# Kernel tuning notes

Measured on AMD Instinct MI355X. Metric: run time of the kernel, lower is better.

The kernel has to match this reference:

```python
import jax, jax.numpy as jnp
import numpy as np

N = 100000       # nodes
E = 1600000      # edges
NFEAT = 128
NHID = 128
NCLASS = 64
NHEAD = 4
NLAYER = 3
LRELU_ALPHA = 0.2


def setup_inputs() -> dict:
    key = jax.random.key(0)
    ks = jax.random.split(key, 7)
    x = jax.random.normal(ks[0], (N, NFEAT), jnp.float32)
    edge_index = jax.random.randint(ks[1], (2, E), 0, N, jnp.int32)
    # xavier-uniform-ish init scales (gain for relu baked into scale roughly)
    Win = jax.random.normal(ks[2], (NFEAT, NHID), jnp.float32) * (2.0 / (NFEAT + NHID)) ** 0.5
    b_in = jnp.zeros((NHID,), jnp.float32)
    # per hidden layer, per head: a split into (src, dst) halves of the (1, 2*in) vector
    a_hid = jax.random.normal(ks[3], (NLAYER - 1, NHEAD, 2, NHID), jnp.float32) * 0.1
    W_hid = jax.random.normal(ks[4], (NLAYER - 1, NHEAD, NHID, NHID // NHEAD), jnp.float32) * (2.0 / (NHID + NHID // NHEAD)) ** 0.5
    a_out = jax.random.normal(ks[5], (2, NHID), jnp.float32) * 0.1
    W_out = jax.random.normal(ks[6], (NHID, NCLASS), jnp.float32) * (2.0 / (NHID + NCLASS)) ** 0.5
    return dict(x=x, edge_index=edge_index, Win=Win, b_in=b_in,
                a_hid=a_hid, W_hid=W_hid, a_out=a_out, W_out=W_out)


def _segment_softmax(logits, seg, n):
    # numerically stable softmax over groups defined by seg (axis 0)
    m = jax.ops.segment_max(logits, seg, num_segments=n)
    e = jnp.exp(logits - m[seg])
    s = jax.ops.segment_sum(e, seg, num_segments=n)
    return e / s[seg]


def _gat_conv(h, row, col, a, W):
    # h: [N, D]; a: [H, 2, D]; W: [H, D, Dh]
    n = h.shape[0]
    H = a.shape[0]
    s_src = h @ a[:, 0, :].T  # [N, H]
    s_dst = h @ a[:, 1, :].T  # [N, H]
    logits = jax.nn.leaky_relu(s_src[row] + s_dst[col], LRELU_ALPHA)  # [E, H]
    alpha = _segment_softmax(logits, row, n)  # softmax grouped by row (edge_index[0])
    h_col = h[col]  # [E, D] gathered once, reused per head
    outs = []
    for hd in range(H):  # small fixed head loop keeps peak memory at [E, D]
        agg = jax.ops.segment_sum(alpha[:, hd, None] * h_col, row, num_segments=n)  # [N, D]
        outs.append(agg @ W[hd])  # weight applied AFTER aggregation, as in source
    return jnp.concatenate(outs, axis=1)


def reference(x, edge_index, Win, b_in, a_hid, W_hid, a_out, W_out):
    row, col = edge_index[0], edge_index[1]
    h = jax.nn.elu(x @ Win + b_in)  # in_linear + ELU (dropout is identity in eval/p=0)
    for l in range(a_hid.shape[0]):
        h = jax.nn.elu(_gat_conv(h, row, col, a_hid[l], W_hid[l]))
    # final conv: single head to nclass, no activation
    return _gat_conv(h, row, col, a_out[None], W_out[None])
```

## Files before the change

kernel.cpp:

```cpp
#include <hip/hip_runtime.h>
#include <hip/hip_bf16.h>
#include <cstdint>
#include <cstddef>

#define LRELU_ALPHA 0.2f
#define LOG2E 1.44269504088896f

typedef __attribute__((ext_vector_type(8))) short short8;
typedef __attribute__((ext_vector_type(4))) float f32x4;
typedef _Float16 h2v __attribute__((ext_vector_type(2)));

__device__ __forceinline__ unsigned short f2bf(float f) {
    unsigned int u = __float_as_uint(f);
    unsigned int r = (u + 0x7fffu + ((u >> 16) & 1u)) >> 16;
    return (unsigned short)r;
}
__device__ __forceinline__ float bf2f(unsigned int lo16) {
    return __uint_as_float(lo16 << 16);
}
__device__ __forceinline__ unsigned int pk2(float a, float b) {
    return (unsigned int)f2bf(a) | ((unsigned int)f2bf(b) << 16);
}
__device__ __forceinline__ float fexp2(float x) {
#if __has_builtin(__builtin_amdgcn_exp2f)
    return __builtin_amdgcn_exp2f(x);
#else
    return __expf(x * 0.69314718056f);
#endif
}
__device__ __forceinline__ h2v pkrtz(float a, float b) {
#if __has_builtin(__builtin_amdgcn_cvt_pkrtz)
    auto r = __builtin_amdgcn_cvt_pkrtz(a, b);
    union { decltype(r) i; h2v o; } u;
    u.i = r;
    return u.o;
#else
    h2v r; r.x = (_Float16)a; r.y = (_Float16)b; return r;
#endif
}
__device__ __forceinline__ unsigned int pack_lo(unsigned int a, unsigned int b) {
#if __has_builtin(__builtin_amdgcn_perm)
    return __builtin_amdgcn_perm(a, b, 0x01000504u);
#else
    return (a & 0xffffu) | (b << 16);
#endif
}
__device__ __forceinline__ unsigned int pack_hi(unsigned int a, unsigned int b) {
#if __has_builtin(__builtin_amdgcn_perm)
    return __builtin_amdgcn_perm(a, b, 0x03020706u);
#else
    return (a >> 16) | (b & 0xffff0000u);
#endif
}
union U32H2 { unsigned int u; h2v h; };
__device__ __forceinline__ float dot2f(unsigned int a, h2v w, float acc) {
    U32H2 c; c.u = a;
#if __has_builtin(__builtin_amdgcn_fdot2)
    return __builtin_amdgcn_fdot2(c.h, w, acc, false);
#else
    return acc + (float)c.h.x * (float)w.x + (float)c.h.y * (float)w.y;
#endif
}


__global__ void fill_hist_k(const int* __restrict__ ei, int* __restrict__ counts,
                            int* __restrict__ rank, int* __restrict__ scol,
                            float* __restrict__ sdA, float* __restrict__ sdB,
                            float* __restrict__ sdC, unsigned int* __restrict__ hW,
                            int N_, int E_, int total) {
    int i = blockIdx.x * 256 + threadIdx.x;
    if (i < total) scol[i] = N_;
    if (i < E_) {
        int r = ei[i];
        rank[i] = atomicAdd(&counts[r], 1);
    }
    if (blockIdx.x == 0) {
        int t = threadIdx.x;
        if (t < 4) { sdA[N_ * 4 + t] = -1e30f; sdB[N_ * 4 + t] = -1e30f; }
        if (t == 4) sdC[N_] = -1e30f;
        if (t >= 32 && t < 64)  hW[(size_t)N_ * 32 + (t - 32)] = 0u;
        if (t >= 64 && t < 128) hW[(size_t)N_ * 64 + (t - 64)] = 0u;
    }
}

__global__ void scan_block_k(const int* __restrict__ counts, int* __restrict__ tmp,
                             int* __restrict__ bsum, int n) {
    __shared__ int s[256];
    int i = blockIdx.x * 256 + threadIdx.x;
    int v = (i < n) ? ((counts[i] + 7) & ~7) : 0;
    s[threadIdx.x] = v;
    __syncthreads();
    for (int d = 1; d < 256; d <<= 1) {
        int t_ = (threadIdx.x >= d) ? s[threadIdx.x - d] : 0;
        __syncthreads();
        s[threadIdx.x] += t_;
        __syncthreads();
    }
    if (i < n) tmp[i] = s[threadIdx.x];
    if (threadIdx.x == 255) bsum[blockIdx.x] = s[255];
}

__global__ void scan_sums_k(int* bsum, int nb) {
    __shared__ int s[512];
    int v = ((int)threadIdx.x < nb) ? bsum[threadIdx.x] : 0;
    s[threadIdx.x] = v;
    __syncthreads();
    for (int d = 1; d < 512; d <<= 1) {
        int t_ = ((int)threadIdx.x >= d) ? s[threadIdx.x - d] : 0;
        __syncthreads();
        s[threadIdx.x] += t_;
        __syncthreads();
    }
    if ((int)threadIdx.x < nb) bsum[threadIdx.x] = s[threadIdx.x] - v;
}

__global__ void finalize_k(const int* __restrict__ tmp, const int* __restrict__ bsum,
                           int* __restrict__ off, int n) {
    int i = blockIdx.x * 256 + threadIdx.x;
    if (i < n) off[i + 1] = tmp[i] + bsum[blockIdx.x];
    if (i == 0) off[0] = 0;
}

__global__ void scatter_k(const int* __restrict__ ei, const int* __restrict__ rank,
                          const int* __restrict__ off, int* __restrict__ scol, int E_) {
    int e = blockIdx.x * 256 + threadIdx.x;
    if (e < E_) {
        int r = ei[e];
        int pos = off[r] + rank[e];
        scol[pos] = ei[E_ + e];
    }
}


__global__ void repack_all(const float* __restrict__ Win, const float* __restrict__ Whid,
                           const float* __restrict__ Wout,
                           unsigned short* __restrict__ W0, unsigned short* __restrict__ W1,
                           unsigned short* __restrict__ W2, unsigned short* __restrict__ W3) {
    int i = blockIdx.x * 256 + threadIdx.x;
    if (i < 16384) {
        int n = i >> 7, k = i & 127;
        W0[i] = f2bf(Win[k * 128 + n]);
    } else if (i < 49152) {
        int j = i - 16384;
        int l = j >> 14;
        int jj = j & 16383;
        int n = jj >> 7, k = jj & 127;
        int hd = n >> 5, c = n & 31;
        float v = Whid[(size_t)l * 16384 + (hd * 128 + k) * 32 + c];
        (l ? W2 : W1)[jj] = f2bf(v);
    } else if (i < 57344) {
        int j = i - 49152;
        int n = j >> 7, k = j & 127;
        W3[j] = f2bf(Wout[k * 64 + n]);
    }
}


template <int KJ, bool ELU_ACT, bool BIAS, int OUTM, bool ABF16>
__global__ __launch_bounds__(256) void gemm_mfma(const void* __restrict__ Xv,
                                                 const unsigned short* __restrict__ WT,
                                                 const float* __restrict__ bias,
                                                 void* __restrict__ Yv, int nRows) {
    constexpr int NT = KJ / 16;
    constexpr int WS = 136;
    __shared__ unsigned short sWT[KJ * WS];
    int t = threadIdx.x;
    for (int i = t; i < KJ * 16; i += 256) {
        int n = i >> 4, k8 = i & 15;
        uint4 v = *(const uint4*)&WT[n * 128 + k8 * 8];
        *(uint4*)&sWT[n * WS + k8 * 8] = v;
    }
    __syncthreads();

    int lane = t & 63;
    int wv = t >> 6;
    int m0 = blockIdx.x * 128 + wv * 32;
    int l16 = lane & 15;
    int q4 = lane >> 4;

    short8 afr[4][2];
    #pragma unroll
    for (int rt = 0; rt < 2; rt++) {
        int row = m0 + rt * 16 + l16;
        bool vr = row < nRows;
        if (ABF16) {
            const unsigned int* xp = (const unsigned int*)Xv + (size_t)row * 64 + q4 * 4;
            #pragma unroll
            for (int kk = 0; kk < 4; kk++) {
                uint4 u = make_uint4(0u, 0u, 0u, 0u);
                if (vr) u = *(const uint4*)(xp + kk * 16);
                afr[kk][rt] = *(short8*)&u;
            }
        } else {
            const float* xp = (const float*)Xv + (size_t)row * 128 + q4 * 8;
            #pragma unroll
            for (int kk = 0; kk < 4; kk++) {
                float4 a0 = make_float4(0.f, 0.f, 0.f, 0.f), a1 = a0;
                if (vr) {
                    a0 = *(const float4*)(xp + kk * 32);
                    a1 = *(const float4*)(xp + kk * 32 + 4);
                }
                unsigned int u[4];
                u[0] = pk2(a0.x, a0.y); u[1] = pk2(a0.z, a0.w);
                u[2] = pk2(a1.x, a1.y); u[3] = pk2(a1.z, a1.w);
                afr[kk][rt] = *(short8*)u;
            }
        }
    }

    f32x4 acc[2][NT] = {};
    #pragma unroll
    for (int kk = 0; kk < 4; kk++) {
        #pragma unroll
        for (int ct = 0; ct < NT; ct++) {
            int n = ct * 16 + l16;
            short8 bf = *(const short8*)&sWT[n * WS + kk * 32 + q4 * 8];
            #pragma unroll
            for (int rt = 0; rt < 2; rt++)
                acc[rt][ct] = __builtin_amdgcn_mfma_f32_16x16x32_bf16(afr[kk][rt], bf, acc[rt][ct], 0, 0, 0);
        }
    }

    #pragma unroll
    for (int rt = 0; rt < 2; rt++) {
        #pragma unroll
        for (int q = 0; q < 4; q++) {
            int row = m0 + rt * 16 + q4 * 4 + q;
            if (row >= nRows) continue;
            #pragma unroll
            for (int ct = 0; ct < NT; ct++) {
                int colc = ct * 16 + l16;
                float v = acc[rt][ct][q];
                if (BIAS) v += bias[colc];
                if (ELU_ACT) v = v > 0.f ? v : (__expf(v) - 1.f);
                if (OUTM == 1) {
                    ((unsigned short*)Yv)[(size_t)row * KJ + colc] = f2bf(v);
                } else if (OUTM == 2) {
                    union { _Float16 hf; unsigned short us; } cv;
                    cv.hf = (_Float16)v;
                    ((unsigned short*)Yv)[(size_t)row * KJ + colc] = cv.us;
                } else {
                    ((float*)Yv)[(size_t)row * KJ + colc] = v;
                }
            }
        }
    }
}


template <int H>
__global__ __launch_bounds__(256) void attn_scores16(const unsigned int* __restrict__ h2,
                                                     const float* __restrict__ a,
                                                     float* __restrict__ s_src,
                                                     float* __restrict__ s_dst, int n) {
    __shared__ float sa[H * 2 * 128];
    for (int i = threadIdx.x; i < H * 2 * 128; i += 256) sa[i] = a[i] * LOG2E;
    __syncthreads();
    int lane = threadIdx.x & 63, wv = threadIdx.x >> 6;
    int sub = lane & 15, g = lane >> 4;
    int node = (blockIdx.x * 4 + wv) * 4 + g;
    bool valid = node < n;
    int nd = valid ? node : 0;
    uint4 hv = *(const uint4*)&h2[(size_t)nd * 64 + sub * 4];
    float f[8];
    f[0] = bf2f(hv.x & 0xffffu); f[1] = bf2f(hv.x >> 16);
    f[2] = bf2f(hv.y & 0xffffu); f[3] = bf2f(hv.y >> 16);
    f[4] = bf2f(hv.z & 0xffffu); f[5] = bf2f(hv.z >> 16);
    f[6] = bf2f(hv.w & 0xffffu); f[7] = bf2f(hv.w >> 16);
    #pragma unroll
    for (int c = 0; c < 2 * H; c++) {
        const float* ap = &sa[c * 128 + sub * 8];
        float p = 0.f;
        #pragma unroll
        for (int q = 0; q < 8; q++) p += f[q] * ap[q];
        #pragma unroll
        for (int s = 1; s < 16; s <<= 1) p += __shfl_xor(p, s);
        if (sub == 0 && valid) {
            float* dst = (c & 1) ? s_dst : s_src;
            dst[node * H + (c >> 1)] = p;
        }
    }
}


template <int DHT, int H, bool ELU_ACT, bool BF16O>
__global__ __launch_bounds__(256) void edge_agg_v(const unsigned int* __restrict__ hW2,
                                                  const float* __restrict__ ssrc,
                                                  const float* __restrict__ sdst,
                                                  const int* __restrict__ off,
                                                  const int* __restrict__ scol,
                                                  void* __restrict__ outv, int nRows) {
    constexpr int FPL = DHT / 16;
    constexpr int UPL = FPL / 2;
    int lane = threadIdx.x & 63;
    int sub = lane & 15;
    int g = lane >> 4;
    int wv = threadIdx.x >> 6;
    int r = __builtin_amdgcn_readfirstlane(blockIdx.x * 4 + wv);
    if (r >= nRows) return;
    int begin = off[r], end = off[r + 1];

    int head = (H == 4) ? (sub >> 2) : 0;
    float ssl = ssrc[r * H + head];

    float acc[FPL] = {};
    float den = 0.f;

    for (int i = begin; i < end; i += 8) {
        int2 cc = *(const int2*)&scol[i + 2 * g];
        int cA = cc.x, cB = cc.y;
        float sdA = sdst[cA * H + head];
        float sdB = sdst[cB * H + head];
        unsigned int hA[UPL], hB[UPL];
        int oA = cA * (DHT / 2) + sub * UPL;
        int oB = cB * (DHT / 2) + sub * UPL;
        if (UPL == 4) {
            *(uint4*)hA = *(const uint4*)&hW2[oA];
            *(uint4*)hB = *(const uint4*)&hW2[oB];
        } else {
            *(uint2*)hA = *(const uint2*)&hW2[oA];
            *(uint2*)hB = *(const uint2*)&hW2[oB];
        }
        float lgA = ssl + sdA;
        float wA = fexp2(fmaxf(lgA, LRELU_ALPHA * lgA));
        float lgB = ssl + sdB;
        float wB = fexp2(fmaxf(lgB, LRELU_ALPHA * lgB));
        den += wA + wB;
        h2v w2 = pkrtz(wA, wB);
        #pragma unroll
        for (int q = 0; q < UPL; q++) {
            acc[2 * q]     = dot2f(pack_lo(hA[q], hB[q]), w2, acc[2 * q]);
            acc[2 * q + 1] = dot2f(pack_hi(hA[q], hB[q]), w2, acc[2 * q + 1]);
        }
    }

    #pragma unroll
    for (int s = 16; s < 64; s <<= 1) {
        den += __shfl_xor(den, s);
        #pragma unroll
        for (int p = 0; p < FPL; p++) acc[p] += __shfl_xor(acc[p], s);
    }
    float inv = den > 0.f ? 1.f / den : 0.f;

    float v[FPL];
    #pragma unroll
    for (int p = 0; p < FPL; p++) {
        float tv = acc[p] * inv;
        if (ELU_ACT) tv = tv > 0.f ? tv : (__expf(tv) - 1.f);
        v[p] = tv;
    }

    if (DHT == 128) {
        if (BF16O)
            ((unsigned int*)outv)[(size_t)r * 64 + sub * 4 + g] = pk2(v[2 * g], v[2 * g + 1]);
        else
            *(float2*)&((float*)outv)[(size_t)r * 128 + sub * 8 + 2 * g] =
                make_float2(v[2 * g], v[2 * g + 1]);
    } else {
        ((float*)outv)[(size_t)r * DHT + sub * FPL + g] = v[g];
    }
}


extern "C" void kernel_launch(void* const* d_in, const int* in_sizes, int n_in,
                              void* d_out, int out_size, void* d_ws, size_t ws_size,
                              hipStream_t stream) {
    const float* x    = (const float*)d_in[0];
    const int*   ei   = (const int*)d_in[1];
    const float* Win  = (const float*)d_in[2];
    const float* bin  = (const float*)d_in[3];
    const float* ahid = (const float*)d_in[4];
    const float* Whid = (const float*)d_in[5];
    const float* aout = (const float*)d_in[6];
    const float* Wout = (const float*)d_in[7];
    float* out = (float*)d_out;

    const int N_ = in_sizes[0] / 128;
    const int E_ = in_sizes[1] / 2;

    char* p = (char*)d_ws;
    auto alloc = [&](size_t bytes) {
        char* q = p;
        p += (bytes + 511) & ~(size_t)511;
        return q;
    };
    int* counts = (int*)alloc((size_t)N_ * 4);
    int* tmp    = (int*)alloc((size_t)N_ * 4);
    int* rank   = (int*)alloc((size_t)E_ * 4);
    int* off    = (int*)alloc((size_t)(N_ + 1) * 4);
    int* bsum   = (int*)alloc(4096);
    int* scol   = (int*)alloc((size_t)(E_ + 8 * N_ + 64) * 4);
    float* ssrcA = (float*)alloc((size_t)(N_ + 1) * 4 * 4);
    float* sdstA = (float*)alloc((size_t)(N_ + 1) * 4 * 4);
    float* ssrcB = (float*)alloc((size_t)(N_ + 1) * 4 * 4);
    float* sdstB = (float*)alloc((size_t)(N_ + 1) * 4 * 4);
    float* ssrcC = (float*)alloc((size_t)(N_ + 1) * 4);
    float* sdstC = (float*)alloc((size_t)(N_ + 1) * 4);
    unsigned int* hb  = (unsigned int*)alloc((size_t)N_ * 64 * 4);
    unsigned int* hWb = (unsigned int*)alloc((size_t)(N_ + 1) * 64 * 4);
    unsigned short* WT0 = (unsigned short*)alloc(128 * 128 * 2);
    unsigned short* WT1 = (unsigned short*)alloc(128 * 128 * 2);
    unsigned short* WT2 = (unsigned short*)alloc(128 * 128 * 2);
    unsigned short* WT3 = (unsigned short*)alloc(64 * 128 * 2);

    int NB = (N_ + 255) / 256;
    int EB = (E_ + 255) / 256;
    int RT = (N_ + 127) / 128;
    int NW = (N_ + 3) / 4;
    int NS = (N_ + 15) / 16;
    int PADTOT = E_ + 8 * N_;

    (void)hipMemsetAsync(counts, 0, (size_t)N_ * 4, stream);
    fill_hist_k<<<(PADTOT + 255) / 256, 256, 0, stream>>>(
        ei, counts, rank, scol, sdstA, sdstB, sdstC, hWb, N_, E_, PADTOT);
    scan_block_k<<<NB, 256, 0, stream>>>(counts, tmp, bsum, N_);
    scan_sums_k<<<1, 512, 0, stream>>>(bsum, NB);
    finalize_k<<<NB, 256, 0, stream>>>(tmp, bsum, off, N_);
    scatter_k<<<EB, 256, 0, stream>>>(ei, rank, off, scol, E_);

    repack_all<<<224, 256, 0, stream>>>(Win, Whid, Wout, WT0, WT1, WT2, WT3);

    gemm_mfma<128, true, true, 1, false><<<RT, 256, 0, stream>>>(x, WT0, bin, hb, N_);

    attn_scores16<4><<<NS, 256, 0, stream>>>(hb, ahid, ssrcA, sdstA, N_);

    gemm_mfma<128, false, false, 2, true><<<RT, 256, 0, stream>>>(hb, WT1, nullptr, hWb, N_);
    edge_agg_v<128, 4, true, true><<<NW, 256, 0, stream>>>(
        hWb, ssrcA, sdstA, off, scol, hb, N_);
    attn_scores16<4><<<NS, 256, 0, stream>>>(hb, ahid + 4 * 2 * 128, ssrcB, sdstB, N_);

    gemm_mfma<128, false, false, 2, true><<<RT, 256, 0, stream>>>(hb, WT2, nullptr, hWb, N_);
    edge_agg_v<128, 4, true, true><<<NW, 256, 0, stream>>>(
        hWb, ssrcB, sdstB, off, scol, hb, N_);
    attn_scores16<1><<<NS, 256, 0, stream>>>(hb, aout, ssrcC, sdstC, N_);

    gemm_mfma<64, false, false, 2, true><<<RT, 256, 0, stream>>>(hb, WT3, nullptr, hWb, N_);
    edge_agg_v<64, 1, false, false><<<NW, 256, 0, stream>>>(
        hWb, ssrcC, sdstC, off, scol, out, N_);
}
```

Measured before the change: 483.5 us.

## Replicate CSR histogram into 8 copies and scatter via atomic cursors

Edge-degree counting now spreads its atomics over 8 replicated count arrays, chosen by block index, so fewer atomics collide on the same counter. The per-edge rank array is dropped: finalize computes a start cursor for each replica and writes the padding entries only for each row's tail, and the scatter claims slots through atomics on those cursors. This removes the full padded fill of scol and the rank read/write, but adds 8x count and cursor arrays, a larger memset, and atomics in the scatter, which also makes the order within each row nondeterministic.

```diff
diff --git a/kernel.cpp b/kernel.cpp
--- a/kernel.cpp
+++ b/kernel.cpp
@@ -63,16 +63,14 @@
 }
 
 
-__global__ void fill_hist_k(const int* __restrict__ ei, int* __restrict__ counts,
-                            int* __restrict__ rank, int* __restrict__ scol,
-                            float* __restrict__ sdA, float* __restrict__ sdB,
-                            float* __restrict__ sdC, unsigned int* __restrict__ hW,
-                            int N_, int E_, int total) {
-    int i = blockIdx.x * 256 + threadIdx.x;
-    if (i < total) scol[i] = N_;
-    if (i < E_) {
-        int r = ei[i];
-        rank[i] = atomicAdd(&counts[r], 1);
+__global__ void hist8_k(const int* __restrict__ ei, int* __restrict__ counts8,
+                        float* __restrict__ sdA, float* __restrict__ sdB,
+                        float* __restrict__ sdC, unsigned int* __restrict__ hW,
+                        int N_, int E_) {
+    int e = blockIdx.x * 256 + threadIdx.x;
+    int rep = blockIdx.x & 7;
+    if (e < E_) {
+        atomicAdd(&counts8[rep * N_ + ei[e]], 1);
     }
     if (blockIdx.x == 0) {
         int t = threadIdx.x;
@@ -83,11 +81,17 @@
     }
 }
 
-__global__ void scan_block_k(const int* __restrict__ counts, int* __restrict__ tmp,
+__global__ void scan_block_k(const int* __restrict__ counts8, int* __restrict__ tmp,
                              int* __restrict__ bsum, int n) {
     __shared__ int s[256];
     int i = blockIdx.x * 256 + threadIdx.x;
-    int v = (i < n) ? ((counts[i] + 7) & ~7) : 0;
+    int v = 0;
+    if (i < n) {
+        int c = 0;
+        #pragma unroll
+        for (int r = 0; r < 8; r++) c += counts8[r * n + i];
+        v = (c + 7) & ~7;
+    }
     s[threadIdx.x] = v;
     __syncthreads();
     for (int d = 1; d < 256; d <<= 1) {
@@ -115,18 +119,31 @@
 }
 
 __global__ void finalize_k(const int* __restrict__ tmp, const int* __restrict__ bsum,
-                           int* __restrict__ off, int n) {
+                           const int* __restrict__ counts8, int* __restrict__ cursor8,
+                           int* __restrict__ off, int* __restrict__ scol, int N_, int n) {
     int i = blockIdx.x * 256 + threadIdx.x;
-    if (i < n) off[i + 1] = tmp[i] + bsum[blockIdx.x];
+    if (i < n) {
+        int end = tmp[i] + bsum[blockIdx.x];
+        off[i + 1] = end;
+        int c[8], cnt = 0;
+        #pragma unroll
+        for (int r = 0; r < 8; r++) { c[r] = counts8[r * n + i]; cnt += c[r]; }
+        int padded = (cnt + 7) & ~7;
+        int pos = end - padded;
+        #pragma unroll
+        for (int r = 0; r < 8; r++) { cursor8[r * n + i] = pos; pos += c[r]; }
+        for (; pos < end; pos++) scol[pos] = N_;
+    }
     if (i == 0) off[0] = 0;
 }
 
-__global__ void scatter_k(const int* __restrict__ ei, const int* __restrict__ rank,
-                          const int* __restrict__ off, int* __restrict__ scol, int E_) {
+__global__ void scatter8_k(const int* __restrict__ ei, int* __restrict__ cursor8,
+                           int* __restrict__ scol, int N_, int E_) {
     int e = blockIdx.x * 256 + threadIdx.x;
+    int rep = blockIdx.x & 7;
     if (e < E_) {
         int r = ei[e];
-        int pos = off[r] + rank[e];
+        int pos = atomicAdd(&cursor8[rep * N_ + r], 1);
         scol[pos] = ei[E_ + e];
     }
 }
@@ -384,12 +401,12 @@
         p += (bytes + 511) & ~(size_t)511;
         return q;
     };
-    int* counts = (int*)alloc((size_t)N_ * 4);
-    int* tmp    = (int*)alloc((size_t)N_ * 4);
-    int* rank   = (int*)alloc((size_t)E_ * 4);
-    int* off    = (int*)alloc((size_t)(N_ + 1) * 4);
-    int* bsum   = (int*)alloc(4096);
-    int* scol   = (int*)alloc((size_t)(E_ + 8 * N_ + 64) * 4);
+    int* counts8 = (int*)alloc((size_t)N_ * 8 * 4);
+    int* cursor8 = (int*)alloc((size_t)N_ * 8 * 4);
+    int* tmp     = (int*)alloc((size_t)N_ * 4);
+    int* off     = (int*)alloc((size_t)(N_ + 1) * 4);
+    int* bsum    = (int*)alloc(4096);
+    int* scol    = (int*)alloc((size_t)(E_ + 8 * N_ + 64) * 4);
     float* ssrcA = (float*)alloc((size_t)(N_ + 1) * 4 * 4);
     float* sdstA = (float*)alloc((size_t)(N_ + 1) * 4 * 4);
     float* ssrcB = (float*)alloc((size_t)(N_ + 1) * 4 * 4);
@@ -408,15 +425,13 @@
     int RT = (N_ + 127) / 128;
     int NW = (N_ + 3) / 4;
     int NS = (N_ + 15) / 16;
-    int PADTOT = E_ + 8 * N_;
-
-    (void)hipMemsetAsync(counts, 0, (size_t)N_ * 4, stream);
-    fill_hist_k<<<(PADTOT + 255) / 256, 256, 0, stream>>>(
-        ei, counts, rank, scol, sdstA, sdstB, sdstC, hWb, N_, E_, PADTOT);
-    scan_block_k<<<NB, 256, 0, stream>>>(counts, tmp, bsum, N_);
+
+    (void)hipMemsetAsync(counts8, 0, (size_t)N_ * 8 * 4, stream);
+    hist8_k<<<EB, 256, 0, stream>>>(ei, counts8, sdstA, sdstB, sdstC, hWb, N_, E_);
+    scan_block_k<<<NB, 256, 0, stream>>>(counts8, tmp, bsum, N_);
     scan_sums_k<<<1, 512, 0, stream>>>(bsum, NB);
-    finalize_k<<<NB, 256, 0, stream>>>(tmp, bsum, off, N_);
-    scatter_k<<<EB, 256, 0, stream>>>(ei, rank, off, scol, E_);
+    finalize_k<<<NB, 256, 0, stream>>>(tmp, bsum, counts8, cursor8, off, scol, N_, N_);
+    scatter8_k<<<EB, 256, 0, stream>>>(ei, cursor8, scol, N_, E_);
 
     repack_all<<<224, 256, 0, stream>>>(Win, Whid, Wout, WT0, WT1, WT2, WT3);
 
```

Result: slower. 583.3 us (+20.6%).
